# Performance work log

Measured on AMD Instinct MI355X. Metric: run time of the kernel, lower is better.

Reference implementation:

```python
import jax, jax.numpy as jnp
import numpy as np

B, N, D_FEAT = 16, 1024, 64
NPOINT, RADIUS, NSAMPLE = 512, 0.2, 32
EPS = 1e-5


def _square_distance(src, dst):
    # src [b,S,3], dst [b,N,3] -> [b,S,N]
    d = -2.0 * jnp.einsum('bsc,bnc->bsn', src, dst)
    d = d + jnp.sum(src * src, -1)[:, :, None]
    d = d + jnp.sum(dst * dst, -1)[:, None, :]
    return d


def _fps(xyz, npoint):
    # xyz [b,N,3] -> indices [b,npoint]; seeded by point farthest from the mean
    b, n, _ = xyz.shape
    centroid = jnp.mean(xyz, axis=1, keepdims=True)
    distance = jnp.minimum(jnp.full((b, n), 1e10, xyz.dtype),
                           jnp.sum((xyz - centroid) ** 2, -1))
    farthest = jnp.argmax(distance, -1)
    bidx = jnp.arange(b)

    def body(carry, _):
        dist, far = carry
        c = xyz[bidx[:, None], far[:, None]]  # [b,1,3]
        dist = jnp.minimum(dist, jnp.sum((xyz - c) ** 2, -1))
        return (dist, jnp.argmax(dist, -1)), far

    _, idx = jax.lax.scan(body, (distance, farthest), None, length=npoint)
    return idx.T  # [b, npoint]


def _gather(points, idx):
    # points [b,N,C], idx [b,...] -> [b,...,C]
    return jax.vmap(lambda p, i: p[i])(points, idx)


def _query_ball(radius, nsample, xyz, new_xyz):
    # faithful to torch: mask out-of-radius with N, full sort, take first nsample,
    # replace sentinels by the first (closest-index) in-ball point
    b, n, _ = xyz.shape
    sqr = _square_distance(new_xyz, xyz)  # [b,S,N]
    idx = jnp.where(sqr > radius ** 2, n, jnp.arange(n)[None, None, :])
    idx = jnp.sort(idx, axis=-1)[:, :, :nsample]
    first = idx[:, :, :1]
    return jnp.where(idx == n, first, idx)


def _qbn(x):
    # QBN_RM training mode: divide by per-channel RMS of detached activations
    mean = jnp.mean(jax.lax.stop_gradient(x) ** 2, axis=(0, 2, 3))
    return x / jnp.sqrt(mean + EPS)[None, :, None, None]


def _qrelu(x):
    # scale each 3-vector by mod / max(mod, 1), coefficient detached
    b3, c, s, k = x.shape
    b = b3 // 3
    xd = jax.lax.stop_gradient(x).reshape(b, 3, c, s, k)
    mod = jnp.sqrt(jnp.sum(xd * xd, axis=1))  # [b,c,s,k]
    coeff = mod / jnp.maximum(mod, 1.0)
    return jnp.broadcast_to(coeff[:, None], (b, 3, c, s, k)).reshape(b3, c, s, k) * x


def _qmaxpool(x):
    # our_mpool1d with kernel (1, nsample): pick the max-modulus sample over K,
    # gather the same index for all 3 quaternion components
    b3, c, s, k = x.shape
    b = b3 // 3
    x5 = x.reshape(b, 3, c, s, k)
    mod = jnp.sum(jax.lax.stop_gradient(x5) ** 2, axis=1)  # argmax of mod == argmax of mod^2
    idx = jnp.argmax(mod, axis=-1)  # [b,c,s]
    idxb = jnp.broadcast_to(idx[:, None, :, :, None], (b, 3, c, s, 1))
    y = jnp.take_along_axis(x5, idxb, axis=-1)[..., 0]  # [b,3,c,s]
    return y.reshape(b3, c, s)


def setup_inputs() -> dict:
    key = jax.random.key(0)
    k1, k2, k3, k4, k5 = jax.random.split(key, 5)
    xyz = jax.random.normal(k1, (B, 3, N), dtype=jnp.float32)
    points = jax.random.normal(k2, (B * 3, D_FEAT, N), dtype=jnp.float32)
    W0 = jax.random.normal(k3, (64, 66), dtype=jnp.float32) * np.sqrt(2.0 / 66)
    W1 = jax.random.normal(k4, (64, 64), dtype=jnp.float32) * np.sqrt(2.0 / 64)
    W2 = jax.random.normal(k5, (128, 64), dtype=jnp.float32) * np.sqrt(2.0 / 64)
    return {"xyz": xyz, "points": points, "W0": W0, "W1": W1, "W2": W2}


def reference(xyz, points, W0, W1, W2):
    xyz_t = xyz.transpose(0, 2, 1)      # [B,N,3]
    pts_t = points.transpose(0, 2, 1)   # [B*3,N,D]

    fps_idx = _fps(xyz_t, NPOINT)                       # [B,S]
    new_xyz = _gather(xyz_t, fps_idx)                   # [B,S,3]
    idx = _query_ball(RADIUS, NSAMPLE, xyz_t, new_xyz)  # [B,S,K]

    g_xyz = _gather(xyz_t, idx)                         # [B,S,K,3]
    g_norm = g_xyz - new_xyz[:, :, None, :]
    gx = g_xyz.transpose(0, 3, 1, 2).reshape(B * 3, NPOINT, NSAMPLE, 1)
    gn = g_norm.transpose(0, 3, 1, 2).reshape(B * 3, NPOINT, NSAMPLE, 1)
    idx3 = jnp.broadcast_to(idx[:, None], (B, 3, NPOINT, NSAMPLE)).reshape(B * 3, NPOINT, NSAMPLE)
    gp = _gather(pts_t, idx3)                           # [B*3,S,K,D]

    x = jnp.concatenate([gn, gx, gp], axis=-1)          # [B*3,S,K,D+2]
    x = x.transpose(0, 3, 1, 2)                         # [B*3,D+2,S,K]
    for W in (W0, W1, W2):
        x = jnp.einsum('bcsk,oc->bosk', x, W)           # 1x1 conv, no bias
        x = _qrelu(_qbn(x))
    new_feat = _qmaxpool(x)                             # [B*3,128,S]
    return new_xyz.transpose(0, 2, 1), new_feat
```

## Files before the change

### kernel.cpp

```cpp
#include <hip/hip_runtime.h>

typedef unsigned int u32;
typedef unsigned long long u64;
typedef float v2f __attribute__((ext_vector_type(2)));

#define NB 16
#define NPT 1024
#define NP 512
#define NS 32
#define DF 64
#define RAD2 0.04f
#define EPSQ 1e-5f
#define CNTF 786432.0f
#define NGRP 8192
#define TCAP 96
#define TSLOT 128
#define NTILE_MAX 2731
#define NHEAT 600
#define NBALLBLK 4096
#define NFILLBLK 1366

__device__ __forceinline__ float rmul(float a, float b){ return __fmul_rn(a,b); }
__device__ __forceinline__ float radd(float a, float b){ return __fadd_rn(a,b); }
__device__ __forceinline__ float sq3(float a, float b, float c){
  return radd(radd(rmul(a,a), rmul(b,b)), rmul(c,c));
}

__device__ __forceinline__ float wave_sum64(float v){
  #pragma unroll
  for(int m=1;m<64;m<<=1) v += __shfl_xor(v, m, 64);
  return v;
}
__device__ __forceinline__ float half_sum32(float v){
  #pragma unroll
  for(int m=1;m<32;m<<=1) v += __shfl_xor(v, m, 64);
  return v;
}

#define DPPK(CTRL) do{ \
  unsigned _lo = (unsigned)k, _hi = (unsigned)(k>>32); \
  unsigned _mlo = (unsigned)__builtin_amdgcn_mov_dpp((int)_lo, (CTRL), 0xF, 0xF, true); \
  unsigned _mhi = (unsigned)__builtin_amdgcn_mov_dpp((int)_hi, (CTRL), 0xF, 0xF, true); \
  u64 _mk = ((u64)_mhi<<32) | _mlo; \
  k = (_mk > k) ? _mk : k; \
}while(0)

template<int PT>
__global__ __launch_bounds__(256) void fps_combo(const float* __restrict__ xyz,
                                                 float* __restrict__ out0,
                                                 const float* __restrict__ pts,
                                                 float* __restrict__ ptsT,
                                                 u32* __restrict__ witem,
                                                 int* __restrict__ idxb_full,
                                                 int* __restrict__ cnt_full,
                                                 int* __restrict__ farIdx,
                                                 int* __restrict__ flagp){
#pragma clang fp contract(off)
  const int bid = blockIdx.x;
  const int t = threadIdx.x;

  if(bid >= 8 + NHEAT){
    if(bid < 8 + NHEAT + NBALLBLK){
      const int row = (bid - 8 - NHEAT)*4 + (t>>6);
      const int lane = t & 63;
      const int b = row >> 10;
      const int nc = row & 1023;
      const float* xb = xyz + b*3*NPT;
      const float s0 = xb[nc], s1 = xb[NPT+nc], s2 = xb[2*NPT+nc];
      const float ss = sq3(s0,s1,s2);
      int base = 0;
      int* rowp = idxb_full + row*NS;
      for(int chk=0; chk<16 && base<NS; ++chk){
        const int n = chk*64 + lane;
        float d0 = xb[n], d1 = xb[NPT+n], d2 = xb[2*NPT+n];
        float dd = sq3(d0,d1,d2);
        float p  = radd(radd(rmul(s0,d0), rmul(s1,d1)), rmul(s2,d2));
        float sqr = radd(radd(rmul(-2.0f,p), ss), dd);
        bool inc = !(sqr > RAD2);
        u64 mask = __ballot(inc);
        if(inc){
          int slot = base + __popcll(mask & ((1ull<<lane)-1ull));
          if(slot < NS) rowp[slot] = n;
        }
        base += __popcll(mask);
      }
      if(lane==0) cnt_full[row] = (base < NS) ? base : NS;
    } else {
      const int gid = (bid - 8 - NHEAT - NBALLBLK)*256 + t;
      if(gid < NTILE_MAX*TSLOT) witem[gid] = 0xFFFFFFFFu;
      if constexpr(PT){
        const int w = gid >> 6, ln = gid & 63;
        if(w < 48*16){
          const int b3 = w >> 4, n0 = (w & 15) << 6;
          const float* src = pts + (((size_t)b3*64 + ln) << 10);
          float* dst = ptsT + (((size_t)b3*1024 + n0) << 6) + ln;
          #pragma unroll 4
          for(int i=0;i<64;i++) dst[(size_t)i << 6] = src[n0 + i];
        }
      }
    }
    return;
  }

  if(bid >= 8){
    if(t >= 64) return;
    __builtin_amdgcn_s_setprio(0);
    const u64 t0 = __builtin_amdgcn_s_memrealtime();
    float a0 = 1.0f, a1 = 1.1f, a2 = 1.2f, a3 = 1.3f;
    while(true){
      #pragma unroll
      for(int i=0;i<128;i++){
        a0 = fmaf(a0, 1.0000001f, 1e-30f);
        a1 = fmaf(a1, 0.9999999f, 1e-30f);
        a2 = fmaf(a2, 1.0000002f, 1e-30f);
        a3 = fmaf(a3, 0.9999998f, 1e-30f);
      }
      if(__hip_atomic_load(flagp, __ATOMIC_RELAXED, __HIP_MEMORY_SCOPE_AGENT) >= 8) break;
      if(__builtin_amdgcn_s_memrealtime() - t0 > 120000ull) break;
    }
    __asm__ volatile("" :: "v"(a0), "v"(a1), "v"(a2), "v"(a3));
    return;
  }

  __shared__ float4 plds[2048];
  if(t >= 64) return;
  __builtin_amdgcn_s_setprio(3);
  const int lane = t;
  const int half = lane >> 5;
  const int hl   = lane & 31;
  const int b    = 2*bid + half;
  const float* xb = xyz + b*3*NPT;

  v2f px2[16], py2[16], pz2[16], dist2[16];
  u32 loj[32];
  #pragma unroll
  for(int i=0;i<16;i++){
    const int n0 = 64*i + hl, n1 = n0 + 32;
    float x0v = xb[n0],        x1v = xb[n1];
    float y0v = xb[NPT+n0],    y1v = xb[NPT+n1];
    float z0v = xb[2*NPT+n0],  z1v = xb[2*NPT+n1];
    px2[i].x = x0v; px2[i].y = x1v;
    py2[i].x = y0v; py2[i].y = y1v;
    pz2[i].x = z0v; pz2[i].y = z1v;
    loj[2*i]   = 1023u - (u32)n0;
    loj[2*i+1] = 1023u - (u32)n1;
    plds[(half<<10) + n0] = make_float4(x0v, y0v, z0v, 0.f);
    plds[(half<<10) + n1] = make_float4(x1v, y1v, z1v, 0.f);
  }
  float sx=0.f, sy=0.f, sz=0.f;
  #pragma unroll
  for(int i=0;i<16;i++){
    sx += px2[i].x; sx += px2[i].y;
    sy += py2[i].x; sy += py2[i].y;
    sz += pz2[i].x; sz += pz2[i].y;
  }
  sx = half_sum32(sx); sy = half_sum32(sy); sz = half_sum32(sz);
  const float cx = sx/1024.f, cy = sy/1024.f, cz = sz/1024.f;
  {
    v2f cx2; cx2.x=cx; cx2.y=cx;
    v2f cy2; cy2.x=cy; cy2.y=cy;
    v2f cz2; cz2.x=cz; cz2.y=cz;
    #pragma unroll
    for(int i=0;i<16;i++){
      v2f dx = px2[i]-cx2, dy = py2[i]-cy2, dz = pz2[i]-cz2;
      v2f m1 = dx*dx, m2 = dy*dy, a1 = m1+m2, m3 = dz*dz, s2 = a1+m3;
      dist2[i].x = fminf(1e10f, s2.x);
      dist2[i].y = fminf(1e10f, s2.y);
    }
  }
  auto reduce2 = [&](int& fA, int& fB){
    u64 kk[16];
    #pragma unroll
    for(int i=0;i<16;i++){
      float a = dist2[i].x, bb = dist2[i].y;
      bool tk = bb > a;
      float dw = tk ? bb : a;
      u32   lw = tk ? loj[2*i+1] : loj[2*i];
      kk[i] = ((u64)__float_as_uint(dw)<<32) | lw;
    }
    #pragma unroll
    for(int i=0;i<8;i++){ u64 l=kk[2*i], r=kk[2*i+1]; kk[i] = (r>l)?r:l; }
    #pragma unroll
    for(int i=0;i<4;i++){ u64 l=kk[2*i], r=kk[2*i+1]; kk[i] = (r>l)?r:l; }
    #pragma unroll
    for(int i=0;i<2;i++){ u64 l=kk[2*i], r=kk[2*i+1]; kk[i] = (r>l)?r:l; }
    u64 k = (kk[1]>kk[0]) ? kk[1] : kk[0];
    DPPK(0xB1);
    DPPK(0x4E);
    DPPK(0x124);
    DPPK(0x128);
    DPPK(0x142);
    unsigned lo = (unsigned)k;
    fA = 1023 - __builtin_amdgcn_readlane((int)lo, 31);
    fB = 1023 - __builtin_amdgcn_readlane((int)lo, 63);
  };

  __asm__ volatile("s_waitcnt lgkmcnt(0)" ::: "memory");
  int farA, farB;
  reduce2(farA, farB);
  for(int it=0; it<NP; ++it){
    const int farv = (lane & 32) ? farB : farA;
    const float4 qv = plds[(half<<10) + farv];
    if(hl == 0){
      out0[(b*3+0)*NP + it] = qv.x;
      out0[(b*3+1)*NP + it] = qv.y;
      out0[(b*3+2)*NP + it] = qv.z;
      farIdx[b*NP + it] = farv;
    }
    v2f qx2; qx2.x=qv.x; qx2.y=qv.x;
    v2f qy2; qy2.x=qv.y; qy2.y=qv.y;
    v2f qz2; qz2.x=qv.z; qz2.y=qv.z;
    #pragma unroll
    for(int i=0;i<16;i++){
      v2f dx = px2[i]-qx2, dy = py2[i]-qy2, dz = pz2[i]-qz2;
      v2f m1 = dx*dx, m2 = dy*dy, a1 = m1+m2, m3 = dz*dz, s2 = a1+m3;
      dist2[i].x = fminf(dist2[i].x, s2.x);
      dist2[i].y = fminf(dist2[i].y, s2.y);
    }
    reduce2(farA, farB);
  }
  if(t == 0) atomicAdd(flagp, 1);
}

__global__ __launch_bounds__(1024) void pack_kernel(const int* __restrict__ farIdx,
                                                    const int* __restrict__ cnt_full,
                                                    const int* __restrict__ idxb_full,
                                                    u32* __restrict__ witem,
                                                    int* __restrict__ ntile_dev,
                                                    int* __restrict__ cntb){
  const int t = threadIdx.x;
  const int lane = t & 63;
  const int wv = t >> 6;
  int c[8]; int rowid[8]; int s0 = 0;
  #pragma unroll
  for(int i=0;i<8;i++){
    const int g = t*8+i;
    const int far = farIdx[g];
    rowid[i] = ((g>>9)<<10) + far;
    c[i] = cnt_full[rowid[i]];
    cntb[g] = c[i];
    s0 += c[i];
  }
  int pre = s0;
  #pragma unroll
  for(int d=1; d<64; d<<=1){
    int v = __shfl_up(pre, d, 64);
    if(lane >= d) pre += v;
  }
  __shared__ int wsum[16];
  if(lane==63) wsum[wv] = pre;
  __syncthreads();
  int wo = 0;
  #pragma unroll
  for(int w=0;w<16;w++) if(w < wv) wo += wsum[w];
  int m = wo + pre - s0;
  if(t==1023) *ntile_dev = (wo + pre + TCAP - 1) / TCAP;
  #pragma unroll
  for(int i=0;i<8;i++){
    const int g = t*8+i; const int cc = c[i];
    const int tile = m / TCAP; const int slot = m - TCAP*tile;
    const int* rp = idxb_full + rowid[i]*NS;
    for(int j=0;j<cc;j++){
      witem[tile*TSLOT + slot + j] = (u32)((g<<15) | (j<<10) | rp[j]);
    }
    m += cc;
  }
}

template<int DEPTH, int PT>
__global__ __launch_bounds__(384) void pass_kernel(
  const float* __restrict__ xyz, const float* __restrict__ ptsrc,
  const float* __restrict__ W0, const float* __restrict__ W1, const float* __restrict__ W2,
  const float* __restrict__ out0, const u32* __restrict__ witem,
  const int* __restrict__ cntb, const int* __restrict__ ntile_dev,
  const float* __restrict__ inv1, const float* __restrict__ inv2,
  float* __restrict__ part, float* __restrict__ out1)
{
  const int t = threadIdx.x;
  const int c3 = t >> 7;
  const int r  = t & 127;
  const int lane = t & 63;
  const int wv = t >> 6;
  const int bi = blockIdx.x;

  if(bi >= *ntile_dev) return;

  __shared__ float sq[3][128][17];
  __shared__ float wstat[6][128];
  for(int i=t; i<6*128; i+=384) (&wstat[0][0])[i] = 0.f;
  __syncthreads();

  const u32 w = witem[bi*TSLOT + r];
  const bool valid = (w != 0xFFFFFFFFu);
  const int bs = valid ? (int)(w >> 15) : 0;
  const int j  = valid ? (int)((w >> 10) & 31) : 1;
  const int n  = valid ? (int)(w & 1023) : 0;
  const int b = bs >> 9;
  const int s = bs & 511;
  const int b3 = b*3 + c3;
  const int cv = cntb[bs];
  const float wgt = valid ? ((j==0) ? (float)(33 - cv) : 1.0f) : 0.0f;

  const float gx = xyz[b3*NPT + n];
  const float cx = out0[b3*NP + s];
  float x0[66];
  x0[0] = gx - cx;
  x0[1] = gx;
  if constexpr(PT){
    const float4* pr4 = reinterpret_cast<const float4*>(ptsrc + (((size_t)b3<<10) + (size_t)n)*DF);
    #pragma unroll
    for(int q=0;q<16;q++){
      float4 v = pr4[q];
      x0[2+4*q] = v.x; x0[3+4*q] = v.y; x0[4+4*q] = v.z; x0[5+4*q] = v.w;
    }
  } else {
    const float* pr = ptsrc + ((size_t)b3*DF)*NPT + n;
    #pragma unroll
    for(int c=0;c<DF;c++) x0[2+c] = pr[(size_t)c*NPT];
  }

  float y1[64];
  #pragma unroll
  for(int ch=0; ch<4; ++ch){
    float acc[16];
    #pragma unroll
    for(int oo=0;oo<16;oo++){
      const int o = ch*16+oo;
      float a = 0.f;
      #pragma unroll
      for(int c=0;c<66;c++) a = fmaf(W0[o*66+c], x0[c], a);
      acc[oo] = a;
    }
    if constexpr(DEPTH == 1){
      #pragma unroll
      for(int oo=0;oo<16;oo++){
        float v = wave_sum64(acc[oo]*acc[oo]*wgt);
        if(lane==0) wstat[wv][ch*16+oo] += v;
      }
    } else {
      #pragma unroll
      for(int oo=0;oo<16;oo++){
        const int o = ch*16+oo;
        float xp = acc[oo] * inv1[o];
        acc[oo] = xp;
        sq[c3][r][oo] = xp*xp;
      }
      __syncthreads();
      #pragma unroll
      for(int oo=0;oo<16;oo++){
        float m2 = (sq[0][r][oo] + sq[1][r][oo]) + sq[2][r][oo];
        float mod = sqrtf(m2);
        float cf = (mod >= 1.f) ? 1.f : mod;
        y1[ch*16+oo] = cf * acc[oo];
      }
      __syncthreads();
    }
  }
  if constexpr(DEPTH == 1){
    __syncthreads();
    if(t < 64){
      float sv = 0.f;
      #pragma unroll
      for(int wq=0;wq<6;wq++) sv += wstat[wq][t];
      part[bi*64 + t] = sv;
    }
    return;
  }

  float y2[64];
  #pragma unroll
  for(int ch=0; ch<4; ++ch){
    float acc[16];
    #pragma unroll
    for(int oo=0;oo<16;oo++){
      const int o = ch*16+oo;
      float a = 0.f;
      #pragma unroll
      for(int c=0;c<64;c++) a = fmaf(W1[o*64+c], y1[c], a);
      acc[oo] = a;
    }
    if constexpr(DEPTH == 2){
      #pragma unroll
      for(int oo=0;oo<16;oo++){
        float v = wave_sum64(acc[oo]*acc[oo]*wgt);
        if(lane==0) wstat[wv][ch*16+oo] += v;
      }
    } else {
      #pragma unroll
      for(int oo=0;oo<16;oo++){
        const int o = ch*16+oo;
        float xp = acc[oo] * inv2[o];
        acc[oo] = xp;
        sq[c3][r][oo] = xp*xp;
      }
      __syncthreads();
      #pragma unroll
      for(int oo=0;oo<16;oo++){
        float m2 = (sq[0][r][oo] + sq[1][r][oo]) + sq[2][r][oo];
        float mod = sqrtf(m2);
        float cf = (mod >= 1.f) ? 1.f : mod;
        y2[ch*16+oo] = cf * acc[oo];
      }
      __syncthreads();
    }
  }
  if constexpr(DEPTH == 2){
    __syncthreads();
    if(t < 64){
      float sv = 0.f;
      #pragma unroll
      for(int wq=0;wq<6;wq++) sv += wstat[wq][t];
      part[bi*64 + t] = sv;
    }
    return;
  }

  #pragma unroll
  for(int ch=0; ch<8; ++ch){
    float a3[16];
    #pragma unroll
    for(int oo=0;oo<16;oo++){
      const int o = ch*16+oo;
      float a = 0.f;
      #pragma unroll
      for(int c=0;c<64;c++) a = fmaf(W2[o*64+c], y2[c], a);
      a3[oo] = a;
      sq[c3][r][oo] = a;
    }
    __syncthreads();
    if(c3 == 0){
      #pragma unroll
      for(int oo=0;oo<16;oo++){
        float a0 = sq[0][r][oo], a1 = sq[1][r][oo], a2 = sq[2][r][oo];
        float m2 = radd(radd(rmul(a0,a0), rmul(a1,a1)), rmul(a2,a2));
        float v = wave_sum64(m2*wgt);
        if(lane==0) wstat[wv][ch*16+oo] += v;
        if(valid && j==0){
          float bvv = m2; int bjj = 0;
          for(int jj=1; jj<cv; ++jj){
            float c0 = sq[0][r+jj][oo], c1 = sq[1][r+jj][oo], c2 = sq[2][r+jj][oo];
            float mm = radd(radd(rmul(c0,c0), rmul(c1,c1)), rmul(c2,c2));
            if(mm > bvv){ bvv = mm; bjj = jj; }
          }
          const int o = ch*16+oo;
          #pragma unroll
          for(int cc=0;cc<3;cc++){
            out1[(((size_t)(3*b+cc))*128 + o)*NP + s] = sq[cc][r+bjj][oo];
          }
        }
      }
    }
    __syncthreads();
  }
  if(t < 128){
    part[bi*128 + t] = wstat[0][t] + wstat[1][t];
  }
}

__global__ __launch_bounds__(256) void fin_kernel(const float* __restrict__ part,
                                                  const int* __restrict__ ntile_dev, int nch,
                                                  float* __restrict__ inv){
  const int o = blockIdx.x;
  const int t = threadIdx.x;
  const int nblk = *ntile_dev;
  float sum = 0.f;
  for(int i=t; i<nblk; i+=256) sum += part[(size_t)i*nch + o];
  sum = wave_sum64(sum);
  __shared__ float red[4];
  if((t&63)==0) red[t>>6] = sum;
  __syncthreads();
  if(t==0){
    float tot = (red[0]+red[1])+(red[2]+red[3]);
    inv[o] = 1.0f / sqrtf(tot/CNTF + EPSQ);
  }
}

__global__ __launch_bounds__(256) void fin3_scale(const float* __restrict__ part3,
                                                  const int* __restrict__ ntile_dev,
                                                  float* __restrict__ out){
  const int o = blockIdx.x;
  const int t = threadIdx.x;
  const int nblk = *ntile_dev;
  float sum = 0.f;
  for(int i=t; i<nblk; i+=256) sum += part3[(size_t)i*128 + o];
  sum = wave_sum64(sum);
  __shared__ float red[4];
  __shared__ float sinv;
  if((t&63)==0) red[t>>6] = sum;
  __syncthreads();
  if(t==0){
    float tot = (red[0]+red[1])+(red[2]+red[3]);
    sinv = 1.0f / sqrtf(tot/CNTF + EPSQ);
  }
  __syncthreads();
  const float iv = sinv;
  float* base = out + NB*3*NP;
  const size_t str = (size_t)128*NP;
  for(int idx=t; idx<NB*NP; idx+=256){
    const int b = idx >> 9, s = idx & 511;
    size_t i0 = ((size_t)(b*3)*128 + o)*NP + s;
    float a0 = base[i0] * iv;
    float a1 = base[i0+str] * iv;
    float a2 = base[i0+2*str] * iv;
    float m2 = (a0*a0 + a1*a1) + a2*a2;
    float mod = sqrtf(m2);
    float cf = (mod >= 1.f) ? 1.f : mod;
    base[i0] = cf*a0; base[i0+str] = cf*a1; base[i0+2*str] = cf*a2;
  }
}

extern "C" void kernel_launch(void* const* d_in, const int* in_sizes, int n_in,
                              void* d_out, int out_size, void* d_ws, size_t ws_size,
                              hipStream_t stream){
  const float* xyz = (const float*)d_in[0];
  const float* pts = (const float*)d_in[1];
  const float* W0  = (const float*)d_in[2];
  const float* W1  = (const float*)d_in[3];
  const float* W2  = (const float*)d_in[4];
  float* out = (float*)d_out;

  char* p = (char*)d_ws;
  auto carve = [&](size_t bytes)->char*{
    char* q = p; p += (bytes + 255) & ~(size_t)255; return q;
  };
  int*   idxb_full = (int*)  carve((size_t)NB*NPT*NS*4);
  int*   cnt_full  = (int*)  carve((size_t)NB*NPT*4);
  int*   farIdx    = (int*)  carve((size_t)NGRP*4);
  int*   flagp     = (int*)  carve(256);
  int*   cntb      = (int*)  carve((size_t)NGRP*4);
  u32*   witem     = (u32*)  carve((size_t)NTILE_MAX*TSLOT*4);
  int*   ntile_dev = (int*)  carve(256);
  float* part1     = (float*)carve((size_t)NTILE_MAX*64*4);
  float* part2     = (float*)carve((size_t)NTILE_MAX*64*4);
  float* part3     = (float*)carve((size_t)NTILE_MAX*128*4);
  float* inv1      = (float*)carve(64*4);
  float* inv2      = (float*)carve(64*4);
  float* inv3      = (float*)carve(128*4);
  size_t base_need = (size_t)(p - (char*)d_ws);
  float* ptsT      = (float*)p;
  const size_t pt_bytes = (size_t)48*1024*64*4;
  const bool use_pt = (ws_size >= base_need + pt_bytes);

  float* out1 = out + NB*3*NP;
  const int nblk = 8 + NHEAT + NBALLBLK + NFILLBLK;

  hipMemsetAsync(flagp, 0, 4, stream);
  if(use_pt) fps_combo<1><<<nblk, 256, 0, stream>>>(xyz, out, pts, ptsT, witem, idxb_full, cnt_full, farIdx, flagp);
  else       fps_combo<0><<<nblk, 256, 0, stream>>>(xyz, out, pts, nullptr, witem, idxb_full, cnt_full, farIdx, flagp);

  pack_kernel<<<1, 1024, 0, stream>>>(farIdx, cnt_full, idxb_full, witem, ntile_dev, cntb);

  if(use_pt){
    pass_kernel<1,1><<<NTILE_MAX, 384, 0, stream>>>(xyz, ptsT, W0, W1, W2, out, witem, cntb, ntile_dev, nullptr, nullptr, part1, nullptr);
    fin_kernel<<<64, 256, 0, stream>>>(part1, ntile_dev, 64, inv1);
    pass_kernel<2,1><<<NTILE_MAX, 384, 0, stream>>>(xyz, ptsT, W0, W1, W2, out, witem, cntb, ntile_dev, inv1, nullptr, part2, nullptr);
    fin_kernel<<<64, 256, 0, stream>>>(part2, ntile_dev, 64, inv2);
    pass_kernel<3,1><<<NTILE_MAX, 384, 0, stream>>>(xyz, ptsT, W0, W1, W2, out, witem, cntb, ntile_dev, inv1, inv2, part3, out1);
  } else {
    pass_kernel<1,0><<<NTILE_MAX, 384, 0, stream>>>(xyz, pts, W0, W1, W2, out, witem, cntb, ntile_dev, nullptr, nullptr, part1, nullptr);
    fin_kernel<<<64, 256, 0, stream>>>(part1, ntile_dev, 64, inv1);
    pass_kernel<2,0><<<NTILE_MAX, 384, 0, stream>>>(xyz, pts, W0, W1, W2, out, witem, cntb, ntile_dev, inv1, nullptr, part2, nullptr);
    fin_kernel<<<64, 256, 0, stream>>>(part2, ntile_dev, 64, inv2);
    pass_kernel<3,0><<<NTILE_MAX, 384, 0, stream>>>(xyz, pts, W0, W1, W2, out, witem, cntb, ntile_dev, inv1, inv2, part3, out1);
  }
  fin3_scale<<<128, 256, 0, stream>>>(part3, ntile_dev, out);
}
```

Before: 789.2 us.

## Cache per-layer conv outputs in workspace across passes and drop heater blocks

Pass 1 stores the first conv layer's pre-norm outputs to a workspace cache, and pass 2 stores the second layer's. Later passes reload these instead of recomputing the earlier matmuls, cutting redundant FMA work but adding global memory traffic of 192 floats per row per layer. The number of cached tiles depends on available workspace, with fallback to recomputation. The spin-loop heater blocks and their completion flag are also removed from the FPS kernel.

New measurement: 749.3 us. 5.1% less time.

```diff
diff --git a/kernel.cpp b/kernel.cpp
--- a/kernel.cpp
+++ b/kernel.cpp
@@ -16,7 +16,6 @@
 #define TCAP 96
 #define TSLOT 128
 #define NTILE_MAX 2731
-#define NHEAT 600
 #define NBALLBLK 4096
 #define NFILLBLK 1366
 
@@ -53,15 +52,14 @@
                                                  u32* __restrict__ witem,
                                                  int* __restrict__ idxb_full,
                                                  int* __restrict__ cnt_full,
-                                                 int* __restrict__ farIdx,
-                                                 int* __restrict__ flagp){
+                                                 int* __restrict__ farIdx){
 #pragma clang fp contract(off)
   const int bid = blockIdx.x;
   const int t = threadIdx.x;
 
-  if(bid >= 8 + NHEAT){
-    if(bid < 8 + NHEAT + NBALLBLK){
-      const int row = (bid - 8 - NHEAT)*4 + (t>>6);
+  if(bid >= 8){
+    if(bid < 8 + NBALLBLK){
+      const int row = (bid - 8)*4 + (t>>6);
       const int lane = t & 63;
       const int b = row >> 10;
       const int nc = row & 1023;
@@ -86,7 +84,7 @@
       }
       if(lane==0) cnt_full[row] = (base < NS) ? base : NS;
     } else {
-      const int gid = (bid - 8 - NHEAT - NBALLBLK)*256 + t;
+      const int gid = (bid - 8 - NBALLBLK)*256 + t;
       if(gid < NTILE_MAX*TSLOT) witem[gid] = 0xFFFFFFFFu;
       if constexpr(PT){
         const int w = gid >> 6, ln = gid & 63;
@@ -99,26 +97,6 @@
         }
       }
     }
-    return;
-  }
-
-  if(bid >= 8){
-    if(t >= 64) return;
-    __builtin_amdgcn_s_setprio(0);
-    const u64 t0 = __builtin_amdgcn_s_memrealtime();
-    float a0 = 1.0f, a1 = 1.1f, a2 = 1.2f, a3 = 1.3f;
-    while(true){
-      #pragma unroll
-      for(int i=0;i<128;i++){
-        a0 = fmaf(a0, 1.0000001f, 1e-30f);
-        a1 = fmaf(a1, 0.9999999f, 1e-30f);
-        a2 = fmaf(a2, 1.0000002f, 1e-30f);
-        a3 = fmaf(a3, 0.9999998f, 1e-30f);
-      }
-      if(__hip_atomic_load(flagp, __ATOMIC_RELAXED, __HIP_MEMORY_SCOPE_AGENT) >= 8) break;
-      if(__builtin_amdgcn_s_memrealtime() - t0 > 120000ull) break;
-    }
-    __asm__ volatile("" :: "v"(a0), "v"(a1), "v"(a2), "v"(a3));
     return;
   }
 
@@ -219,7 +197,6 @@
     }
     reduce2(farA, farB);
   }
-  if(t == 0) atomicAdd(flagp, 1);
 }
 
 __global__ __launch_bounds__(1024) void pack_kernel(const int* __restrict__ farIdx,
@@ -274,7 +251,8 @@
   const float* __restrict__ out0, const u32* __restrict__ witem,
   const int* __restrict__ cntb, const int* __restrict__ ntile_dev,
   const float* __restrict__ inv1, const float* __restrict__ inv2,
-  float* __restrict__ part, float* __restrict__ out1)
+  float* __restrict__ part, float* __restrict__ out1,
+  int cache_tiles, float* __restrict__ cacheA, float* __restrict__ cacheB)
 {
   const int t = threadIdx.x;
   const int c3 = t >> 7;
@@ -284,6 +262,9 @@
   const int bi = blockIdx.x;
 
   if(bi >= *ntile_dev) return;
+  const bool use_cache = (bi < cache_tiles);
+  float* cslotA = cacheA + ((size_t)bi*TSLOT + r)*192 + (size_t)c3*64;
+  float* cslotB = cacheB + ((size_t)bi*TSLOT + r)*192 + (size_t)c3*64;
 
   __shared__ float sq[3][128][17];
   __shared__ float wstat[6][128];
@@ -301,62 +282,123 @@
   const int cv = cntb[bs];
   const float wgt = valid ? ((j==0) ? (float)(33 - cv) : 1.0f) : 0.0f;
 
-  const float gx = xyz[b3*NPT + n];
-  const float cx = out0[b3*NP + s];
-  float x0[66];
-  x0[0] = gx - cx;
-  x0[1] = gx;
-  if constexpr(PT){
-    const float4* pr4 = reinterpret_cast<const float4*>(ptsrc + (((size_t)b3<<10) + (size_t)n)*DF);
+  float acc64[64];
+  if(DEPTH >= 2 && use_cache){
     #pragma unroll
     for(int q=0;q<16;q++){
-      float4 v = pr4[q];
-      x0[2+4*q] = v.x; x0[3+4*q] = v.y; x0[4+4*q] = v.z; x0[5+4*q] = v.w;
+      float4 v = ((const float4*)cslotA)[q];
+      acc64[4*q]=v.x; acc64[4*q+1]=v.y; acc64[4*q+2]=v.z; acc64[4*q+3]=v.w;
     }
   } else {
-    const float* pr = ptsrc + ((size_t)b3*DF)*NPT + n;
-    #pragma unroll
-    for(int c=0;c<DF;c++) x0[2+c] = pr[(size_t)c*NPT];
+    const float gx = xyz[b3*NPT + n];
+    const float cx = out0[b3*NP + s];
+    float x0[66];
+    x0[0] = gx - cx;
+    x0[1] = gx;
+    if constexpr(PT){
+      const float4* pr4 = reinterpret_cast<const float4*>(ptsrc + (((size_t)b3<<10) + (size_t)n)*DF);
+      #pragma unroll
+      for(int q=0;q<16;q++){
+        float4 v = pr4[q];
+        x0[2+4*q] = v.x; x0[3+4*q] = v.y; x0[4+4*q] = v.z; x0[5+4*q] = v.w;
+      }
+    } else {
+      const float* pr = ptsrc + ((size_t)b3*DF)*NPT + n;
+      #pragma unroll
+      for(int c=0;c<DF;c++) x0[2+c] = pr[(size_t)c*NPT];
+    }
+    #pragma unroll
+    for(int ch=0; ch<4; ++ch){
+      #pragma unroll
+      for(int oo=0;oo<16;oo++){
+        const int o = ch*16+oo;
+        float a = 0.f;
+        #pragma unroll
+        for(int c=0;c<66;c++) a = fmaf(W0[o*66+c], x0[c], a);
+        acc64[o] = a;
+      }
+    }
+    if(DEPTH == 1 && use_cache){
+      #pragma unroll
+      for(int q=0;q<16;q++){
+        float4 v; v.x=acc64[4*q]; v.y=acc64[4*q+1]; v.z=acc64[4*q+2]; v.w=acc64[4*q+3];
+        ((float4*)cslotA)[q] = v;
+      }
+    }
+  }
+
+  if constexpr(DEPTH == 1){
+    #pragma unroll
+    for(int o=0;o<64;o++){
+      float v = wave_sum64(acc64[o]*acc64[o]*wgt);
+      if(lane==0) wstat[wv][o] += v;
+    }
+    __syncthreads();
+    if(t < 64){
+      float sv = 0.f;
+      #pragma unroll
+      for(int wq=0;wq<6;wq++) sv += wstat[wq][t];
+      part[bi*64 + t] = sv;
+    }
+    return;
   }
 
   float y1[64];
   #pragma unroll
   for(int ch=0; ch<4; ++ch){
-    float acc[16];
+    float xp16[16];
     #pragma unroll
     for(int oo=0;oo<16;oo++){
       const int o = ch*16+oo;
-      float a = 0.f;
-      #pragma unroll
-      for(int c=0;c<66;c++) a = fmaf(W0[o*66+c], x0[c], a);
-      acc[oo] = a;
-    }
-    if constexpr(DEPTH == 1){
-      #pragma unroll
-      for(int oo=0;oo<16;oo++){
-        float v = wave_sum64(acc[oo]*acc[oo]*wgt);
-        if(lane==0) wstat[wv][ch*16+oo] += v;
-      }
-    } else {
+      float xp = acc64[o] * inv1[o];
+      xp16[oo] = xp;
+      sq[c3][r][oo] = xp*xp;
+    }
+    __syncthreads();
+    #pragma unroll
+    for(int oo=0;oo<16;oo++){
+      float m2 = (sq[0][r][oo] + sq[1][r][oo]) + sq[2][r][oo];
+      float mod = sqrtf(m2);
+      float cf = (mod >= 1.f) ? 1.f : mod;
+      y1[ch*16+oo] = cf * xp16[oo];
+    }
+    __syncthreads();
+  }
+
+  float acc2[64];
+  if(DEPTH == 3 && use_cache){
+    #pragma unroll
+    for(int q=0;q<16;q++){
+      float4 v = ((const float4*)cslotB)[q];
+      acc2[4*q]=v.x; acc2[4*q+1]=v.y; acc2[4*q+2]=v.z; acc2[4*q+3]=v.w;
+    }
+  } else {
+    #pragma unroll
+    for(int ch=0; ch<4; ++ch){
       #pragma unroll
       for(int oo=0;oo<16;oo++){
         const int o = ch*16+oo;
-        float xp = acc[oo] * inv1[o];
-        acc[oo] = xp;
-        sq[c3][r][oo] = xp*xp;
-      }
-      __syncthreads();
-      #pragma unroll
-      for(int oo=0;oo<16;oo++){
-        float m2 = (sq[0][r][oo] + sq[1][r][oo]) + sq[2][r][oo];
-        float mod = sqrtf(m2);
-        float cf = (mod >= 1.f) ? 1.f : mod;
-        y1[ch*16+oo] = cf * acc[oo];
-      }
-      __syncthreads();
-    }
-  }
-  if constexpr(DEPTH == 1){
+        float a = 0.f;
+        #pragma unroll
+        for(int c=0;c<64;c++) a = fmaf(W1[o*64+c], y1[c], a);
+        acc2[o] = a;
+      }
+    }
+    if(DEPTH == 2 && use_cache){
+      #pragma unroll
+      for(int q=0;q<16;q++){
+        float4 v; v.x=acc2[4*q]; v.y=acc2[4*q+1]; v.z=acc2[4*q+2]; v.w=acc2[4*q+3];
+        ((float4*)cslotB)[q] = v;
+      }
+    }
+  }
+
+  if constexpr(DEPTH == 2){
+    #pragma unroll
+    for(int o=0;o<64;o++){
+      float v = wave_sum64(acc2[o]*acc2[o]*wgt);
+      if(lane==0) wstat[wv][o] += v;
+    }
     __syncthreads();
     if(t < 64){
       float sv = 0.f;
@@ -370,49 +412,23 @@
   float y2[64];
   #pragma unroll
   for(int ch=0; ch<4; ++ch){
-    float acc[16];
+    float xp16[16];
     #pragma unroll
     for(int oo=0;oo<16;oo++){
       const int o = ch*16+oo;
-      float a = 0.f;
-      #pragma unroll
-      for(int c=0;c<64;c++) a = fmaf(W1[o*64+c], y1[c], a);
-      acc[oo] = a;
-    }
-    if constexpr(DEPTH == 2){
-      #pragma unroll
-      for(int oo=0;oo<16;oo++){
-        float v = wave_sum64(acc[oo]*acc[oo]*wgt);
-        if(lane==0) wstat[wv][ch*16+oo] += v;
-      }
-    } else {
-      #pragma unroll
-      for(int oo=0;oo<16;oo++){
-        const int o = ch*16+oo;
-        float xp = acc[oo] * inv2[o];
-        acc[oo] = xp;
-        sq[c3][r][oo] = xp*xp;
-      }
-      __syncthreads();
-      #pragma unroll
-      for(int oo=0;oo<16;oo++){
-        float m2 = (sq[0][r][oo] + sq[1][r][oo]) + sq[2][r][oo];
-        float mod = sqrtf(m2);
-        float cf = (mod >= 1.f) ? 1.f : mod;
-        y2[ch*16+oo] = cf * acc[oo];
-      }
-      __syncthreads();
-    }
-  }
-  if constexpr(DEPTH == 2){
-    __syncthreads();
-    if(t < 64){
-      float sv = 0.f;
-      #pragma unroll
-      for(int wq=0;wq<6;wq++) sv += wstat[wq][t];
-      part[bi*64 + t] = sv;
-    }
-    return;
+      float xp = acc2[o] * inv2[o];
+      xp16[oo] = xp;
+      sq[c3][r][oo] = xp*xp;
+    }
+    __syncthreads();
+    #pragma unroll
+    for(int oo=0;oo<16;oo++){
+      float m2 = (sq[0][r][oo] + sq[1][r][oo]) + sq[2][r][oo];
+      float mod = sqrtf(m2);
+      float cf = (mod >= 1.f) ? 1.f : mod;
+      y2[ch*16+oo] = cf * xp16[oo];
+    }
+    __syncthreads();
   }
 
   #pragma unroll
@@ -526,7 +542,6 @@
   int*   idxb_full = (int*)  carve((size_t)NB*NPT*NS*4);
   int*   cnt_full  = (int*)  carve((size_t)NB*NPT*4);
   int*   farIdx    = (int*)  carve((size_t)NGRP*4);
-  int*   flagp     = (int*)  carve(256);
   int*   cntb      = (int*)  carve((size_t)NGRP*4);
   u32*   witem     = (u32*)  carve((size_t)NTILE_MAX*TSLOT*4);
   int*   ntile_dev = (int*)  carve(256);
@@ -539,29 +554,37 @@
   size_t base_need = (size_t)(p - (char*)d_ws);
   float* ptsT      = (float*)p;
   const size_t pt_bytes = (size_t)48*1024*64*4;
-  const bool use_pt = (ws_size >= base_need + pt_bytes);
+  const bool use_pt = (ws_size >= base_need + pt_bytes + (1u<<20));
+
+  size_t fixed = base_need + (use_pt ? pt_bytes : 0);
+  const size_t per_tile = (size_t)TSLOT*192*4*2;
+  int cache_tiles = 0;
+  if(ws_size > fixed + per_tile)
+    cache_tiles = (int)(((ws_size - fixed) / per_tile));
+  if(cache_tiles > NTILE_MAX) cache_tiles = NTILE_MAX;
+  float* cacheA = (float*)((char*)d_ws + fixed);
+  float* cacheB = cacheA + (size_t)cache_tiles*TSLOT*192;
 
   float* out1 = out + NB*3*NP;
-  const int nblk = 8 + NHEAT + NBALLBLK + NFILLBLK;
-
-  hipMemsetAsync(flagp, 0, 4, stream);
-  if(use_pt) fps_combo<1><<<nblk, 256, 0, stream>>>(xyz, out, pts, ptsT, witem, idxb_full, cnt_full, farIdx, flagp);
-  else       fps_combo<0><<<nblk, 256, 0, stream>>>(xyz, out, pts, nullptr, witem, idxb_full, cnt_full, farIdx, flagp);
+  const int nblk = 8 + NBALLBLK + NFILLBLK;
+
+  if(use_pt) fps_combo<1><<<nblk, 256, 0, stream>>>(xyz, out, pts, ptsT, witem, idxb_full, cnt_full, farIdx);
+  else       fps_combo<0><<<nblk, 256, 0, stream>>>(xyz, out, pts, nullptr, witem, idxb_full, cnt_full, farIdx);
 
   pack_kernel<<<1, 1024, 0, stream>>>(farIdx, cnt_full, idxb_full, witem, ntile_dev, cntb);
 
   if(use_pt){
-    pass_kernel<1,1><<<NTILE_MAX, 384, 0, stream>>>(xyz, ptsT, W0, W1, W2, out, witem, cntb, ntile_dev, nullptr, nullptr, part1, nullptr);
+    pass_kernel<1,1><<<NTILE_MAX, 384, 0, stream>>>(xyz, ptsT, W0, W1, W2, out, witem, cntb, ntile_dev, nullptr, nullptr, part1, nullptr, cache_tiles, cacheA, cacheB);
     fin_kernel<<<64, 256, 0, stream>>>(part1, ntile_dev, 64, inv1);
-    pass_kernel<2,1><<<NTILE_MAX, 384, 0, stream>>>(xyz, ptsT, W0, W1, W2, out, witem, cntb, ntile_dev, inv1, nullptr, part2, nullptr);
+    pass_kernel<2,1><<<NTILE_MAX, 384, 0, stream>>>(xyz, ptsT, W0, W1, W2, out, witem, cntb, ntile_dev, inv1, nullptr, part2, nullptr, cache_tiles, cacheA, cacheB);
     fin_kernel<<<64, 256, 0, stream>>>(part2, ntile_dev, 64, inv2);
-    pass_kernel<3,1><<<NTILE_MAX, 384, 0, stream>>>(xyz, ptsT, W0, W1, W2, out, witem, cntb, ntile_dev, inv1, inv2, part3, out1);
+    pass_kernel<3,1><<<NTILE_MAX, 384, 0, stream>>>(xyz, ptsT, W0, W1, W2, out, witem, cntb, ntile_dev, inv1, inv2, part3, out1, cache_tiles, cacheA, cacheB);
   } else {
-    pass_kernel<1,0><<<NTILE_MAX, 384, 0, stream>>>(xyz, pts, W0, W1, W2, out, witem, cntb, ntile_dev, nullptr, nullptr, part1, nullptr);
+    pass_kernel<1,0><<<NTILE_MAX, 384, 0, stream>>>(xyz, pts, W0, W1, W2, out, witem, cntb, ntile_dev, nullptr, nullptr, part1, nullptr, cache_tiles, cacheA, cacheB);
     fin_kernel<<<64, 256, 0, stream>>>(part1, ntile_dev, 64, inv1);
-    pass_kernel<2,0><<<NTILE_MAX, 384, 0, stream>>>(xyz, pts, W0, W1, W2, out, witem, cntb, ntile_dev, inv1, nullptr, part2, nullptr);
+    pass_kernel<2,0><<<NTILE_MAX, 384, 0, stream>>>(xyz, pts, W0, W1, W2, out, witem, cntb, ntile_dev, inv1, nullptr, part2, nullptr, cache_tiles, cacheA, cacheB);
     fin_kernel<<<64, 256, 0, stream>>>(part2, ntile_dev, 64, inv2);
-    pass_kernel<3,0><<<NTILE_MAX, 384, 0, stream>>>(xyz, pts, W0, W1, W2, out, witem, cntb, ntile_dev, inv1, inv2, part3, out1);
+    pass_kernel<3,0><<<NTILE_MAX, 384, 0, stream>>>(xyz, pts, W0, W1, W2, out, witem, cntb, ntile_dev, inv1, inv2, part3, out1, cache_tiles, cacheA, cacheB);
   }
   fin3_scale<<<128, 256, 0, stream>>>(part3, ntile_dev, out);
 }
```
